# Kernel tuning notes

Measured on AMD Instinct MI355X. Metric: run time of the kernel, lower is better.

## Reference

```python
import jax, jax.numpy as jnp
import numpy as np

L = 32768          # sequence length (keys/values)
E = 1024           # embed_dim (hardcoded in module via weight slices)
H, D = 8, 128      # num_heads, head_dim (hardcoded via reshape(-1, 8, 128))


def setup_inputs() -> dict:
    key = jax.random.key(0)
    k1, k2, k3, k4, k5 = jax.random.split(key, 5)
    scale = 1.0 / np.sqrt(E)
    return {
        "x": jax.random.normal(k1, (L, E), dtype=jnp.float32),
        "in_proj_weight": jax.random.normal(k2, (3 * E, E), dtype=jnp.float32) * scale,
        "in_proj_bias": jax.random.normal(k3, (3 * E,), dtype=jnp.float32) * 0.02,
        "out_proj_weight": jax.random.normal(k4, (E, E), dtype=jnp.float32) * scale,
        "out_proj_bias": jax.random.normal(k5, (E,), dtype=jnp.float32) * 0.02,
    }


def reference(x, in_proj_weight, in_proj_bias, out_proj_weight, out_proj_bias):
    # Single-query (decode-style) attention: q from first token only.
    q = x[:1] @ in_proj_weight[:E].T + in_proj_bias[:E]              # [1, E]
    k = x @ in_proj_weight[E:2 * E].T + in_proj_bias[E:2 * E]        # [L, E]
    v = x @ in_proj_weight[2 * E:].T + in_proj_bias[2 * E:]          # [L, E]

    q = q.reshape(-1, H, D).transpose(1, 0, 2)                       # [H, 1, D]
    k = k.reshape(-1, H, D).transpose(1, 2, 0)                       # [H, D, L]
    v = v.reshape(-1, H, D).transpose(1, 0, 2)                       # [H, L, D]

    dot = jnp.matmul(q, k) * (1.0 / np.sqrt(D))                      # [H, 1, L]
    attn = jax.nn.softmax(dot, axis=-1)
    out = jnp.matmul(attn, v)                                        # [H, 1, D]

    out = out.transpose(1, 0, 2).reshape(-1, E)                      # [1, E]
    out = out @ out_proj_weight.T + out_proj_bias                    # [1, E]
    return out
```

## Files before the change

### kernel.cpp

```cpp
#include <hip/hip_runtime.h>
#include <math.h>


#define L_SEQ   32768
#define E_DIM   1024
#define NHEAD   8
#define HDIM    128
#define TILE_R  8
#define WAVES_M 8

__global__ __launch_bounds__(256) void proj_q(
    const float* __restrict__ W, const float* __restrict__ bias,
    const float* __restrict__ x, float* __restrict__ q)
{
  const int t = threadIdx.x, wave = t >> 6, lane = t & 63;
  const int o = blockIdx.x * 4 + wave;
  const float4* Wr = (const float4*)(W + (size_t)o * E_DIM);
  const float4* xr = (const float4*)x;
  float a = 0.f;
#pragma unroll
  for (int k = 0; k < 4; ++k) {
    float4 wv = Wr[lane + 64 * k];
    float4 xv = xr[lane + 64 * k];
    a += wv.x * xv.x + wv.y * xv.y + wv.z * xv.z + wv.w * xv.w;
  }
#pragma unroll
  for (int m = 1; m < 64; m <<= 1) a += __shfl_xor(a, m, 64);
  if (lane == 0) q[o] = a + bias[o];
}

__global__ __launch_bounds__(128) void make_p(
    const float* __restrict__ W, const float* __restrict__ q,
    float* __restrict__ P_T)
{
  const int h = blockIdx.y;
  const int e = blockIdx.x * 128 + threadIdx.x;
  const float* qh = q + h * HDIM;
  const float* Wb = W + ((size_t)E_DIM + (size_t)h * HDIM) * E_DIM + e;
  float a0 = 0.f, a1 = 0.f, a2 = 0.f, a3 = 0.f;
#pragma unroll 4
  for (int d = 0; d < HDIM; d += 4) {
    a0 += qh[d + 0] * Wb[(size_t)(d + 0) * E_DIM];
    a1 += qh[d + 1] * Wb[(size_t)(d + 1) * E_DIM];
    a2 += qh[d + 2] * Wb[(size_t)(d + 2) * E_DIM];
    a3 += qh[d + 3] * Wb[(size_t)(d + 3) * E_DIM];
  }
  P_T[h * E_DIM + e] = ((a0 + a1) + (a2 + a3)) * 0.08838834764831845f;
}

__global__ __launch_bounds__(512, 2) void attn_fused4(
    const float* __restrict__ x,
    const float* __restrict__ P_T,
    float* __restrict__ partial_z,
    float* __restrict__ partial_sumw,
    int rows_per_blk)
{
  __shared__ __align__(16) float P_lds[NHEAD * E_DIM];
  __shared__ __align__(16) float x_tile[TILE_R][E_DIM];
  __shared__ __align__(16) float w_tile[TILE_R][NHEAD];
  __shared__ __align__(16) float sw_stage[WAVES_M][NHEAD];

  const int t = threadIdx.x;
  const int wave = t >> 6;
  const int lane = t & 63;
  const size_t row0 = (size_t)blockIdx.x * rows_per_blk;
  const int ntiles = rows_per_blk / TILE_R;

  const int h_l = ((lane & 1) << 2) | (((lane >> 1) & 1) << 1) | ((lane >> 2) & 1);

  {
    const float4* src = (const float4*)P_T;
    float4* dst = (float4*)P_lds;
#pragma unroll
    for (int i = 0; i < 4; ++i) dst[i * 512 + t] = src[i * 512 + t];
  }
  __syncthreads();

  float acc[16];
#pragma unroll
  for (int i = 0; i < 16; ++i) acc[i] = 0.f;
  float sumw_own = 0.f;

  float4 xv[4];
  {
    const float4* xr = (const float4*)(x + (row0 + wave) * E_DIM);
#pragma unroll
    for (int k = 0; k < 4; ++k) xv[k] = xr[lane + 64 * k];
  }

  for (int tile = 0; tile < ntiles; ++tile) {
    const size_t trow = row0 + (size_t)tile * TILE_R;

    {
      float4* xd = (float4*)&x_tile[wave][0];
#pragma unroll
      for (int k = 0; k < 4; ++k) xd[lane + 64 * k] = xv[k];
    }

    float4 xn[4];
    if (tile + 1 < ntiles) {
      const float4* xr = (const float4*)(x + (trow + TILE_R + wave) * E_DIM);
#pragma unroll
      for (int k = 0; k < 4; ++k) xn[k] = xr[lane + 64 * k];
    }

    float v[NHEAD];
#pragma unroll
    for (int h = 0; h < NHEAD; ++h) {
      const float4* pr = (const float4*)(P_lds + h * E_DIM);
      float a = 0.f;
#pragma unroll
      for (int k = 0; k < 4; ++k) {
        float4 p = pr[lane + 64 * k];
        a += xv[k].x * p.x + xv[k].y * p.y + xv[k].z * p.z + xv[k].w * p.w;
      }
      v[h] = a;
    }

#pragma unroll
    for (int lev = 0; lev < 3; ++lev) {
      const int d = 1 << lev;
      const int half = 4 >> lev;
#pragma unroll
      for (int i = 0; i < half; ++i) {
        float lo = v[i], hi = v[i + half];
        float keep = (lane & d) ? hi : lo;
        float oth  = (lane & d) ? lo : hi;
        v[i] = keep + __shfl_xor(oth, d, 64);
      }
    }
    float tot = v[0];
    tot += __shfl_xor(tot, 8, 64);
    tot += __shfl_xor(tot, 16, 64);
    tot += __shfl_xor(tot, 32, 64);

    const float w = __expf(tot);
    sumw_own += w;
    if (lane < 8) w_tile[wave][h_l] = w;

    __syncthreads();

#pragma unroll
    for (int r = 0; r < TILE_R; ++r) {
      const float2 xv2 = *(const float2*)&x_tile[r][2 * t];
      const float4* wp = (const float4*)&w_tile[r][0];
      const float4 wlo = wp[0], whi = wp[1];
      acc[0]  += wlo.x * xv2.x;  acc[1]  += wlo.x * xv2.y;
      acc[2]  += wlo.y * xv2.x;  acc[3]  += wlo.y * xv2.y;
      acc[4]  += wlo.z * xv2.x;  acc[5]  += wlo.z * xv2.y;
      acc[6]  += wlo.w * xv2.x;  acc[7]  += wlo.w * xv2.y;
      acc[8]  += whi.x * xv2.x;  acc[9]  += whi.x * xv2.y;
      acc[10] += whi.y * xv2.x;  acc[11] += whi.y * xv2.y;
      acc[12] += whi.z * xv2.x;  acc[13] += whi.z * xv2.y;
      acc[14] += whi.w * xv2.x;  acc[15] += whi.w * xv2.y;
    }

    __syncthreads();

    if (tile + 1 < ntiles) {
#pragma unroll
      for (int k = 0; k < 4; ++k) xv[k] = xn[k];
    }
  }

  {
    float* zd = partial_z + (size_t)blockIdx.x * (NHEAD * E_DIM) + 2 * t;
#pragma unroll
    for (int h = 0; h < NHEAD; ++h)
      *(float2*)(zd + h * E_DIM) = make_float2(acc[2 * h], acc[2 * h + 1]);
  }

  if (lane < 8) sw_stage[wave][h_l] = sumw_own;
  __syncthreads();
  if (t < NHEAD) {
    float s = 0.f;
#pragma unroll
    for (int wv = 0; wv < WAVES_M; ++wv) s += sw_stage[wv][t];
    partial_sumw[blockIdx.x * NHEAD + t] = s;
  }
}

__global__ __launch_bounds__(256) void reduce_z(
    const float* __restrict__ partial_z,
    const float* __restrict__ partial_sumw,
    float* __restrict__ zn, int nblk)
{
  __shared__ float red[256];
  __shared__ __align__(16) float swst[4][NHEAD];
  __shared__ float sumw_s[NHEAD];
  const int t = threadIdx.x;
  const int lane = t & 63, wave = t >> 6;

  float sw[NHEAD];
#pragma unroll
  for (int h = 0; h < NHEAD; ++h) sw[h] = 0.f;
  for (int b = t; b < nblk; b += 256) {
    const float4* p = (const float4*)(partial_sumw + (size_t)b * NHEAD);
    float4 a0 = p[0], a1 = p[1];
    sw[0] += a0.x; sw[1] += a0.y; sw[2] += a0.z; sw[3] += a0.w;
    sw[4] += a1.x; sw[5] += a1.y; sw[6] += a1.z; sw[7] += a1.w;
  }
#pragma unroll
  for (int m = 1; m < 64; m <<= 1) {
#pragma unroll
    for (int h = 0; h < NHEAD; ++h) sw[h] += __shfl_xor(sw[h], m, 64);
  }
  if (lane == 0) {
#pragma unroll
    for (int h = 0; h < NHEAD; ++h) swst[wave][h] = sw[h];
  }
  __syncthreads();
  if (t < NHEAD) sumw_s[t] = swst[0][t] + swst[1][t] + swst[2][t] + swst[3][t];

  const int o = blockIdx.x * 32 + (t & 31);
  const int g = t >> 5;
  float a = 0.f;
  for (int b = g; b < nblk; b += 8) a += partial_z[(size_t)b * (NHEAD * E_DIM) + o];
  red[t] = a;
  __syncthreads();
  if (t < 32) {
    float s2 = 0.f;
#pragma unroll
    for (int gg = 0; gg < 8; ++gg) s2 += red[gg * 32 + t];
    const int oo = blockIdx.x * 32 + t;
    zn[oo] = s2 / sumw_s[oo >> 10];
  }
}

__global__ __launch_bounds__(256) void proj_v(
    const float* __restrict__ W, const float* __restrict__ bias,
    const float* __restrict__ zn, float* __restrict__ attn)
{
  const int t = threadIdx.x, wave = t >> 6, lane = t & 63;
  const int o = blockIdx.x * 4 + wave;
  const float4* Wr = (const float4*)(W + ((size_t)2 * E_DIM + o) * E_DIM);
  const float4* zr = (const float4*)(zn + (size_t)(o >> 7) * E_DIM);
  float a = 0.f;
#pragma unroll
  for (int k = 0; k < 4; ++k) {
    float4 wv = Wr[lane + 64 * k];
    float4 zv = zr[lane + 64 * k];
    a += wv.x * zv.x + wv.y * zv.y + wv.z * zv.z + wv.w * zv.w;
  }
#pragma unroll
  for (int m = 1; m < 64; m <<= 1) a += __shfl_xor(a, m, 64);
  if (lane == 0) attn[o] = a + bias[2 * E_DIM + o];
}

__global__ __launch_bounds__(256) void proj_o(
    const float* __restrict__ Wo, const float* __restrict__ bo,
    const float* __restrict__ attn, float* __restrict__ out)
{
  const int t = threadIdx.x, wave = t >> 6, lane = t & 63;
  const int o = blockIdx.x * 4 + wave;
  const float4* Wr = (const float4*)(Wo + (size_t)o * E_DIM);
  const float4* vr = (const float4*)attn;
  float a = 0.f;
#pragma unroll
  for (int k = 0; k < 4; ++k) {
    float4 wv = Wr[lane + 64 * k];
    float4 vv = vr[lane + 64 * k];
    a += wv.x * vv.x + wv.y * vv.y + wv.z * vv.z + wv.w * vv.w;
  }
#pragma unroll
  for (int m = 1; m < 64; m <<= 1) a += __shfl_xor(a, m, 64);
  if (lane == 0) out[o] = a + bo[o];
}

extern "C" void kernel_launch(void* const* d_in, const int* in_sizes, int n_in,
                              void* d_out, int out_size, void* d_ws, size_t ws_size,
                              hipStream_t stream)
{
  const float* x  = (const float*)d_in[0];
  const float* Wi = (const float*)d_in[1];
  const float* bi = (const float*)d_in[2];
  const float* Wo = (const float*)d_in[3];
  const float* bo = (const float*)d_in[4];
  float* out = (float*)d_out;

  char* ws = (char*)d_ws;
  float* q     = (float*)(ws + 0);
  float* P_T   = (float*)(ws + 4096);
  float* zn    = (float*)(ws + 36864);
  float* attn  = (float*)(ws + 69632);
  float* psumw = (float*)(ws + 73728);
  const size_t pz_off = 90112;
  float* pz    = (float*)(ws + pz_off);

  int nblk = 128;
  if (ws_size >= pz_off + (size_t)512 * NHEAD * E_DIM * 4) nblk = 512;
  else if (ws_size >= pz_off + (size_t)256 * NHEAD * E_DIM * 4) nblk = 256;
  const int rows_per_blk = L_SEQ / nblk;

  proj_q     <<<256, 256, 0, stream>>>(Wi, bi, x, q);
  make_p     <<<dim3(8, 8), 128, 0, stream>>>(Wi, q, P_T);
  attn_fused4<<<nblk, 512, 0, stream>>>(x, P_T, pz, psumw, rows_per_blk);
  reduce_z   <<<256, 256, 0, stream>>>(pz, psumw, zn, nblk);
  proj_v     <<<256, 256, 0, stream>>>(Wi, bi, zn, attn);
  proj_o     <<<256, 256, 0, stream>>>(Wo, bo, attn, out);
}
```

Baseline: 241.3 us.

## Double-buffer x tiles via direct global-to-LDS loads and split heads across waves

The main attention kernel now stages x rows into a double-buffered LDS tile using global_load_lds, which avoids a round trip through registers. Each wave now owns two heads and half of the tile rows, keeping its P rows and z accumulators in registers. This replaces the shared P table and the per-tile weight exchange, removing one barrier per tile. The make_p kernel is also restructured to use float4 loads with an in-block reduction over d groups. The cost is higher register pressure and a final cross-wave reduction through LDS.

```diff
diff --git a/kernel.cpp b/kernel.cpp
--- a/kernel.cpp
+++ b/kernel.cpp
@@ -9,6 +9,11 @@
 #define TILE_R  8
 #define WAVES_M 8
 
+#define GLD16(gp, lp)                                                   \
+  __builtin_amdgcn_global_load_lds(                                     \
+      (const __attribute__((address_space(1))) void*)(gp),              \
+      (__attribute__((address_space(3))) void*)(lp), 16, 0, 0)
+
 __global__ __launch_bounds__(256) void proj_q(
     const float* __restrict__ W, const float* __restrict__ bias,
     const float* __restrict__ x, float* __restrict__ q)
@@ -29,155 +34,153 @@
   if (lane == 0) q[o] = a + bias[o];
 }
 
-__global__ __launch_bounds__(128) void make_p(
+__global__ __launch_bounds__(256) void make_p(
     const float* __restrict__ W, const float* __restrict__ q,
     float* __restrict__ P_T)
 {
-  const int h = blockIdx.y;
-  const int e = blockIdx.x * 128 + threadIdx.x;
-  const float* qh = q + h * HDIM;
-  const float* Wb = W + ((size_t)E_DIM + (size_t)h * HDIM) * E_DIM + e;
-  float a0 = 0.f, a1 = 0.f, a2 = 0.f, a3 = 0.f;
-#pragma unroll 4
-  for (int d = 0; d < HDIM; d += 4) {
-    a0 += qh[d + 0] * Wb[(size_t)(d + 0) * E_DIM];
-    a1 += qh[d + 1] * Wb[(size_t)(d + 1) * E_DIM];
-    a2 += qh[d + 2] * Wb[(size_t)(d + 2) * E_DIM];
-    a3 += qh[d + 3] * Wb[(size_t)(d + 3) * E_DIM];
-  }
-  P_T[h * E_DIM + e] = ((a0 + a1) + (a2 + a3)) * 0.08838834764831845f;
-}
-
-__global__ __launch_bounds__(512, 2) void attn_fused4(
+  __shared__ __align__(16) float4 ps[8][32];
+  const int t  = threadIdx.x;
+  const int h  = blockIdx.y;
+  const int ec = blockIdx.x;
+  const int eg = t & 31;
+  const int dg = t >> 5;
+  const float* Wb = W + ((size_t)E_DIM + h * HDIM + dg * 16) * E_DIM + ec * 128 + eg * 4;
+  const float* qh = q + h * HDIM + dg * 16;
+  float4 a = make_float4(0.f, 0.f, 0.f, 0.f);
+#pragma unroll
+  for (int dd = 0; dd < 16; ++dd) {
+    const float qv = qh[dd];
+    const float4 wv = *(const float4*)(Wb + (size_t)dd * E_DIM);
+    a.x += qv * wv.x; a.y += qv * wv.y; a.z += qv * wv.z; a.w += qv * wv.w;
+  }
+  ps[dg][eg] = a;
+  __syncthreads();
+  if (t < 32) {
+    float4 s = ps[0][t];
+#pragma unroll
+    for (int g = 1; g < 8; ++g) {
+      const float4 b = ps[g][t];
+      s.x += b.x; s.y += b.y; s.z += b.z; s.w += b.w;
+    }
+    const float sc = 0.08838834764831845f;
+    s.x *= sc; s.y *= sc; s.z *= sc; s.w *= sc;
+    *(float4*)(P_T + (size_t)h * E_DIM + ec * 128 + t * 4) = s;
+  }
+}
+
+__global__ __launch_bounds__(512, 2) void attn_fused5(
     const float* __restrict__ x,
     const float* __restrict__ P_T,
     float* __restrict__ partial_z,
     float* __restrict__ partial_sumw,
     int rows_per_blk)
 {
-  __shared__ __align__(16) float P_lds[NHEAD * E_DIM];
-  __shared__ __align__(16) float x_tile[TILE_R][E_DIM];
-  __shared__ __align__(16) float w_tile[TILE_R][NHEAD];
-  __shared__ __align__(16) float sw_stage[WAVES_M][NHEAD];
-
-  const int t = threadIdx.x;
+  __shared__ __align__(16) float sbuf[2][TILE_R][E_DIM];
+  __shared__ float swst[16];
+
+  const int t    = threadIdx.x;
   const int wave = t >> 6;
   const int lane = t & 63;
+  const int rh   = wave >> 2;
+  const int h0   = (wave & 3) * 2;
   const size_t row0 = (size_t)blockIdx.x * rows_per_blk;
-  const int ntiles = rows_per_blk / TILE_R;
-
-  const int h_l = ((lane & 1) << 2) | (((lane >> 1) & 1) << 1) | ((lane >> 2) & 1);
-
+  const int ntiles  = rows_per_blk / TILE_R;
+
+  float4 p0[4], p1[4];
   {
-    const float4* src = (const float4*)P_T;
-    float4* dst = (float4*)P_lds;
-#pragma unroll
-    for (int i = 0; i < 4; ++i) dst[i * 512 + t] = src[i * 512 + t];
-  }
-  __syncthreads();
-
-  float acc[16];
-#pragma unroll
-  for (int i = 0; i < 16; ++i) acc[i] = 0.f;
-  float sumw_own = 0.f;
-
-  float4 xv[4];
+    const float4* P0 = (const float4*)(P_T + (size_t)h0 * E_DIM);
+    const float4* P1 = (const float4*)(P_T + (size_t)(h0 + 1) * E_DIM);
+#pragma unroll
+    for (int k = 0; k < 4; ++k) { p0[k] = P0[64 * k + lane]; p1[k] = P1[64 * k + lane]; }
+  }
+
+  float4 z0[4], z1[4];
+#pragma unroll
+  for (int k = 0; k < 4; ++k) {
+    z0[k] = make_float4(0.f, 0.f, 0.f, 0.f);
+    z1[k] = make_float4(0.f, 0.f, 0.f, 0.f);
+  }
+  float sumw0 = 0.f, sumw1 = 0.f;
+
   {
-    const float4* xr = (const float4*)(x + (row0 + wave) * E_DIM);
-#pragma unroll
-    for (int k = 0; k < 4; ++k) xv[k] = xr[lane + 64 * k];
-  }
+    const float* g = x + (row0 + wave) * E_DIM + 4 * lane;
+#pragma unroll
+    for (int k = 0; k < 4; ++k) GLD16(g + k * 256, &sbuf[0][wave][k * 256]);
+  }
+  __syncthreads();
 
   for (int tile = 0; tile < ntiles; ++tile) {
-    const size_t trow = row0 + (size_t)tile * TILE_R;
-
-    {
-      float4* xd = (float4*)&x_tile[wave][0];
-#pragma unroll
-      for (int k = 0; k < 4; ++k) xd[lane + 64 * k] = xv[k];
+    const int buf = tile & 1;
+
+    if (tile + 1 < ntiles) {
+      const float* g = x + (row0 + (size_t)(tile + 1) * TILE_R + wave) * E_DIM + 4 * lane;
+#pragma unroll
+      for (int k = 0; k < 4; ++k) GLD16(g + k * 256, &sbuf[buf ^ 1][wave][k * 256]);
     }
 
-    float4 xn[4];
-    if (tile + 1 < ntiles) {
-      const float4* xr = (const float4*)(x + (trow + TILE_R + wave) * E_DIM);
-#pragma unroll
-      for (int k = 0; k < 4; ++k) xn[k] = xr[lane + 64 * k];
-    }
-
-    float v[NHEAD];
-#pragma unroll
-    for (int h = 0; h < NHEAD; ++h) {
-      const float4* pr = (const float4*)(P_lds + h * E_DIM);
-      float a = 0.f;
+#pragma unroll
+    for (int rl = 0; rl < 4; ++rl) {
+      const float4* xr4 = (const float4*)&sbuf[buf][rh * 4 + rl][0];
+      float4 xr[4];
+#pragma unroll
+      for (int k = 0; k < 4; ++k) xr[k] = xr4[64 * k + lane];
+
+      float s0 = 0.f, s1 = 0.f;
 #pragma unroll
       for (int k = 0; k < 4; ++k) {
-        float4 p = pr[lane + 64 * k];
-        a += xv[k].x * p.x + xv[k].y * p.y + xv[k].z * p.z + xv[k].w * p.w;
+        s0 += xr[k].x * p0[k].x + xr[k].y * p0[k].y + xr[k].z * p0[k].z + xr[k].w * p0[k].w;
+        s1 += xr[k].x * p1[k].x + xr[k].y * p1[k].y + xr[k].z * p1[k].z + xr[k].w * p1[k].w;
       }
-      v[h] = a;
-    }
-
-#pragma unroll
-    for (int lev = 0; lev < 3; ++lev) {
-      const int d = 1 << lev;
-      const int half = 4 >> lev;
-#pragma unroll
-      for (int i = 0; i < half; ++i) {
-        float lo = v[i], hi = v[i + half];
-        float keep = (lane & d) ? hi : lo;
-        float oth  = (lane & d) ? lo : hi;
-        v[i] = keep + __shfl_xor(oth, d, 64);
+
+      const bool odd = (lane & 1);
+      float keep = odd ? s1 : s0;
+      float oth  = odd ? s0 : s1;
+      float ts = keep + __shfl_xor(oth, 1, 64);
+      ts += __shfl_xor(ts, 2, 64);
+      ts += __shfl_xor(ts, 4, 64);
+      ts += __shfl_xor(ts, 8, 64);
+      ts += __shfl_xor(ts, 16, 64);
+      ts += __shfl_xor(ts, 32, 64);
+      const float ex = __expf(ts);
+      const float ox = __shfl_xor(ex, 1, 64);
+      const float w0 = odd ? ox : ex;
+      const float w1 = odd ? ex : ox;
+      sumw0 += w0; sumw1 += w1;
+
+#pragma unroll
+      for (int k = 0; k < 4; ++k) {
+        z0[k].x += w0 * xr[k].x; z0[k].y += w0 * xr[k].y;
+        z0[k].z += w0 * xr[k].z; z0[k].w += w0 * xr[k].w;
+        z1[k].x += w1 * xr[k].x; z1[k].y += w1 * xr[k].y;
+        z1[k].z += w1 * xr[k].z; z1[k].w += w1 * xr[k].w;
       }
     }
-    float tot = v[0];
-    tot += __shfl_xor(tot, 8, 64);
-    tot += __shfl_xor(tot, 16, 64);
-    tot += __shfl_xor(tot, 32, 64);
-
-    const float w = __expf(tot);
-    sumw_own += w;
-    if (lane < 8) w_tile[wave][h_l] = w;
 
     __syncthreads();
-
-#pragma unroll
-    for (int r = 0; r < TILE_R; ++r) {
-      const float2 xv2 = *(const float2*)&x_tile[r][2 * t];
-      const float4* wp = (const float4*)&w_tile[r][0];
-      const float4 wlo = wp[0], whi = wp[1];
-      acc[0]  += wlo.x * xv2.x;  acc[1]  += wlo.x * xv2.y;
-      acc[2]  += wlo.y * xv2.x;  acc[3]  += wlo.y * xv2.y;
-      acc[4]  += wlo.z * xv2.x;  acc[5]  += wlo.z * xv2.y;
-      acc[6]  += wlo.w * xv2.x;  acc[7]  += wlo.w * xv2.y;
-      acc[8]  += whi.x * xv2.x;  acc[9]  += whi.x * xv2.y;
-      acc[10] += whi.y * xv2.x;  acc[11] += whi.y * xv2.y;
-      acc[12] += whi.z * xv2.x;  acc[13] += whi.z * xv2.y;
-      acc[14] += whi.w * xv2.x;  acc[15] += whi.w * xv2.y;
+  }
+
+  float (*zs)[E_DIM] = (float(*)[E_DIM])&sbuf[0][0][0];
+  {
+    float4* zd0 = (float4*)&zs[2 * wave][0];
+    float4* zd1 = (float4*)&zs[2 * wave + 1][0];
+#pragma unroll
+    for (int k = 0; k < 4; ++k) { zd0[64 * k + lane] = z0[k]; zd1[64 * k + lane] = z1[k]; }
+  }
+  if (lane == 0) { swst[2 * wave] = sumw0; swst[2 * wave + 1] = sumw1; }
+  __syncthreads();
+
+  {
+    const float4* zsv = (const float4*)&zs[0][0];
+    float4* pzb = (float4*)(partial_z + (size_t)blockIdx.x * (NHEAD * E_DIM));
+#pragma unroll
+    for (int j = 0; j < 4; ++j) {
+      const int idx = t + 512 * j;
+      const float4 a = zsv[idx], b = zsv[idx + 2048];
+      pzb[idx] = make_float4(a.x + b.x, a.y + b.y, a.z + b.z, a.w + b.w);
     }
-
-    __syncthreads();
-
-    if (tile + 1 < ntiles) {
-#pragma unroll
-      for (int k = 0; k < 4; ++k) xv[k] = xn[k];
-    }
-  }
-
-  {
-    float* zd = partial_z + (size_t)blockIdx.x * (NHEAD * E_DIM) + 2 * t;
-#pragma unroll
-    for (int h = 0; h < NHEAD; ++h)
-      *(float2*)(zd + h * E_DIM) = make_float2(acc[2 * h], acc[2 * h + 1]);
-  }
-
-  if (lane < 8) sw_stage[wave][h_l] = sumw_own;
-  __syncthreads();
-  if (t < NHEAD) {
-    float s = 0.f;
-#pragma unroll
-    for (int wv = 0; wv < WAVES_M; ++wv) s += sw_stage[wv][t];
-    partial_sumw[blockIdx.x * NHEAD + t] = s;
-  }
+  }
+  if (t < NHEAD)
+    partial_sumw[blockIdx.x * NHEAD + t] = swst[t] + swst[t + 8];
 }
 
 __global__ __launch_bounds__(256) void reduce_z(
@@ -293,8 +296,8 @@
   const int rows_per_blk = L_SEQ / nblk;
 
   proj_q     <<<256, 256, 0, stream>>>(Wi, bi, x, q);
-  make_p     <<<dim3(8, 8), 128, 0, stream>>>(Wi, q, P_T);
-  attn_fused4<<<nblk, 512, 0, stream>>>(x, P_T, pz, psumw, rows_per_blk);
+  make_p     <<<dim3(8, 8), 256, 0, stream>>>(Wi, q, P_T);
+  attn_fused5<<<nblk, 512, 0, stream>>>(x, P_T, pz, psumw, rows_per_blk);
   reduce_z   <<<256, 256, 0, stream>>>(pz, psumw, zn, nblk);
   proj_v     <<<256, 256, 0, stream>>>(Wi, bi, zn, attn);
   proj_o     <<<256, 256, 0, stream>>>(Wo, bo, attn, out);
```

Measured after the change: 242.6 us. Within noise of the previous version (+0.5%).
